# Kernel optimization log

Measured on AMD Instinct MI355X. Metric: run time of the kernel, lower is better.

The kernel has to match this reference:

```python
import jax, jax.numpy as jnp
import numpy as np


def _silu(x):
    return x * jax.nn.sigmoid(x)


def _mamba_dir(h, W_in, conv_w, conv_b, Wx, Wdt, bdt, A_log, Dp, W_out):
    """One unidirectional Mamba (v1) block. h: [B, L, Dm] -> [B, L, Dm]."""
    Bsz, L, Dm = h.shape
    Di = W_in.shape[0] // 2
    N = A_log.shape[1]
    K = conv_w.shape[1]
    dt_rank = Wdt.shape[1]
    # input projection -> x, z gates
    xz = jnp.einsum('bld,ed->ble', h, W_in)  # [B, L, 2*Di]
    x, z = xz[..., :Di], xz[..., Di:]
    # causal depthwise conv over time
    xc = jnp.transpose(x, (0, 2, 1))  # [B, Di, L]
    xc = jax.lax.conv_general_dilated(
        xc, conv_w[:, None, :], window_strides=(1,), padding=[(K - 1, 0)],
        dimension_numbers=('NCH', 'OIH', 'NCH'), feature_group_count=Di)
    x = _silu(jnp.transpose(xc, (0, 2, 1)) + conv_b[None, None, :])  # [B, L, Di]
    # data-dependent dt, B, C
    x_dbl = jnp.einsum('bld,ed->ble', x, Wx)  # [B, L, dt_rank + 2N]
    dt = x_dbl[..., :dt_rank]
    Bm = x_dbl[..., dt_rank:dt_rank + N]      # [B, L, N]
    Cm = x_dbl[..., dt_rank + N:]             # [B, L, N]
    dt = jax.nn.softplus(jnp.einsum('blr,dr->bld', dt, Wdt) + bdt)  # [B, L, Di]
    A = -jnp.exp(A_log)                       # [Di, N]
    # ZOH discretization
    dA = jnp.exp(dt[..., None] * A)                     # [B, L, Di, N]
    dBx = (dt * x)[..., None] * Bm[:, :, None, :]       # [B, L, Di, N]

    def step(hc, inp):
        dA_t, dBx_t, C_t = inp
        hc = dA_t * hc + dBx_t                          # [B, Di, N]
        return hc, jnp.einsum('bdn,bn->bd', hc, C_t)

    h0 = jnp.zeros((Bsz, Di, N), dtype=x.dtype)
    _, ys = jax.lax.scan(step, h0, (jnp.moveaxis(dA, 1, 0),
                                    jnp.moveaxis(dBx, 1, 0),
                                    jnp.moveaxis(Cm, 1, 0)))
    y = jnp.moveaxis(ys, 0, 1) + x * Dp                  # [B, L, Di]
    y = y * _silu(z)
    return jnp.einsum('bld,ed->ble', y, W_out)           # [B, L, Dm]


def setup_inputs() -> dict:
    key = jax.random.key(0)
    ks = jax.random.split(key, 16)
    B, L, Dm = 1, 2048, 1024
    Di, N, Kc, R = 2048, 16, 4, 64
    s = 0.02
    inp = {
        'hidden_states': jax.random.normal(ks[0], (B, L, Dm), jnp.float32),
        'W_in':  jax.random.normal(ks[1], (2 * Di, Dm), jnp.float32) * s,
        'W_out': jax.random.normal(ks[2], (Dm, Di), jnp.float32) * s,
    }
    a_log = jnp.log(jnp.broadcast_to(jnp.arange(1, N + 1, dtype=jnp.float32), (Di, N)))
    for i, d in enumerate(['fwd', 'rev']):
        o = 3 + 6 * i
        inp[f'conv_w_{d}'] = jax.random.normal(ks[o + 0], (Di, Kc), jnp.float32) * 0.2
        inp[f'conv_b_{d}'] = jnp.zeros((Di,), jnp.float32)
        inp[f'Wx_{d}']     = jax.random.normal(ks[o + 1], (R + 2 * N, Di), jnp.float32) * s
        inp[f'Wdt_{d}']    = jax.random.normal(ks[o + 2], (Di, R), jnp.float32) * s
        inp[f'bdt_{d}']    = jnp.full((Di,), -4.6, jnp.float32)  # softplus ~ 0.01
        inp[f'A_log_{d}']  = a_log
        inp[f'D_{d}']      = jnp.ones((Di,), jnp.float32)
    return inp


def reference(hidden_states, W_in, W_out,
              conv_w_fwd, conv_b_fwd, Wx_fwd, Wdt_fwd, bdt_fwd, A_log_fwd, D_fwd,
              conv_w_rev, conv_b_rev, Wx_rev, Wdt_rev, bdt_rev, A_log_rev, D_rev):
    out = _mamba_dir(hidden_states, W_in, conv_w_fwd, conv_b_fwd, Wx_fwd,
                     Wdt_fwd, bdt_fwd, A_log_fwd, D_fwd, W_out)
    h_rev = jnp.flip(hidden_states, axis=-2)
    out_rev = _mamba_dir(h_rev, W_in, conv_w_rev, conv_b_rev, Wx_rev,
                         Wdt_rev, bdt_rev, A_log_rev, D_rev, W_out)
    return out + jnp.flip(out_rev, axis=-2)
```

## Files before the change

kernel.cpp:

```cpp
#include <hip/hip_runtime.h>

#define L_LEN 2048
#define DM 1024
#define DI 2048
#define NS 16
#define KC 4
#define RR 64
#define XS 128
#define SPK 8
#define CH2 64
#define TCH2 (L_LEN / CH2)

typedef __attribute__((ext_vector_type(8))) short bf16x8;
typedef __attribute__((ext_vector_type(4))) float f32x4;

__device__ __forceinline__ float silu_f(float v) { return v / (1.f + __expf(-v)); }

__device__ __forceinline__ unsigned short f2bf(float f) {
  unsigned int u = __float_as_uint(f);
  u = (u + 0x7FFFu + ((u >> 16) & 1u)) >> 16;
  return (unsigned short)u;
}
__device__ __forceinline__ float bf2f(unsigned short u) {
  return __uint_as_float((unsigned int)u << 16);
}

#define GLOAD_LDS16(gptr, lptr)                                                \
  __builtin_amdgcn_global_load_lds(                                            \
      (const __attribute__((address_space(1))) void*)(gptr),                   \
      (__attribute__((address_space(3))) void*)(lptr), 16, 0, 0)

template <int BM, int EPI, int KSPLIT>
__global__ __launch_bounds__(256) void gemm_bf16(
    const unsigned short* __restrict__ A, const unsigned short* __restrict__ B,
    void* __restrict__ Cv, void* __restrict__ Cv2, int M, int N, int K,
    size_t zsA, size_t zsB, size_t zsC,
    const float* __restrict__ biasf, const float* __restrict__ biasr)
{
  constexpr int MF = BM / 32;
  constexpr int WM = BM / 2;
  A += (size_t)blockIdx.z * zsA;
  B += (size_t)blockIdx.z * zsB;
  __shared__ unsigned short smem[(BM + 128) * 32];
  unsigned short* As = smem;
  unsigned short* Bs = smem + BM * 32;
  const int tid = threadIdx.x;
  const int wid = tid >> 6;
  const int lane = tid & 63;
  const int bm = blockIdx.x * BM;
  const int bn = (KSPLIT > 1) ? 0 : blockIdx.y * 128;
  int kbeg = 0, kend = K;
  if (KSPLIT > 1) {
    int kl = K / KSPLIT;
    kbeg = blockIdx.y * kl; kend = kbeg + kl;
  }
  const int wm = wid >> 1, wn = wid & 1;
  const int arow = tid >> 2;
  const int swz_kel = (((tid & 3) ^ ((tid >> 3) & 3)) << 3);
  const int qa = (((lane >> 4) ^ ((lane >> 1) & 3)) << 4);
  const int frow = lane & 15;

  f32x4 acc[MF][4];
#pragma unroll
  for (int mi = 0; mi < MF; ++mi)
#pragma unroll
    for (int ni = 0; ni < 4; ++ni) acc[mi][ni] = 0.f;

  const unsigned short* Ab = A + (size_t)bm * K + swz_kel;
  const unsigned short* Bb = B + (size_t)bn * K + swz_kel;

  for (int k0 = kbeg; k0 < kend; k0 += 32) {
#pragma unroll
    for (int i = 0; i < BM / 64; ++i)
      GLOAD_LDS16(Ab + (size_t)(i * 64 + arow) * K + k0,
                  (char*)As + i * 4096 + wid * 1024);
#pragma unroll
    for (int i = 0; i < 2; ++i)
      GLOAD_LDS16(Bb + (size_t)(i * 64 + arow) * K + k0,
                  (char*)Bs + i * 4096 + wid * 1024);
    __syncthreads();
    bf16x8 af[MF], bfr[4];
#pragma unroll
    for (int mi = 0; mi < MF; ++mi)
      af[mi] = *(const bf16x8*)((const char*)As + (wm * WM + mi * 16 + frow) * 64 + qa);
#pragma unroll
    for (int ni = 0; ni < 4; ++ni)
      bfr[ni] = *(const bf16x8*)((const char*)Bs + (wn * 64 + ni * 16 + frow) * 64 + qa);
#pragma unroll
    for (int mi = 0; mi < MF; ++mi)
#pragma unroll
      for (int ni = 0; ni < 4; ++ni)
        acc[mi][ni] = __builtin_amdgcn_mfma_f32_16x16x32_bf16(
            af[mi], bfr[ni], acc[mi][ni], 0, 0, 0);
    __syncthreads();
  }
  const int crow0 = bm + wm * WM + ((lane >> 4) << 2);
  const int ccol0 = bn + wn * 64 + frow;
  if (EPI == 1) {
    unsigned short* Cu = (unsigned short*)Cv + (size_t)blockIdx.z * zsC;
    const float* bias = blockIdx.z ? biasr : biasf;
    float bn4[4];
#pragma unroll
    for (int ni = 0; ni < 4; ++ni) bn4[ni] = bias[ccol0 + ni * 16];
#pragma unroll
    for (int mi = 0; mi < MF; ++mi)
#pragma unroll
      for (int ni = 0; ni < 4; ++ni)
#pragma unroll
        for (int v = 0; v < 4; ++v) {
          float val = acc[mi][ni][v] + bn4[ni];
          float sp = (val > 20.f) ? val : __logf(1.f + __expf(val));
          Cu[(size_t)(crow0 + mi * 16 + v) * N + ccol0 + ni * 16] = f2bf(sp);
        }
  } else if (EPI == 2) {
    unsigned short* Co = (bn < DI) ? (unsigned short*)Cv : (unsigned short*)Cv2;
    const int cbase = (bn < DI) ? 0 : DI;
#pragma unroll
    for (int mi = 0; mi < MF; ++mi)
#pragma unroll
      for (int ni = 0; ni < 4; ++ni)
#pragma unroll
        for (int v = 0; v < 4; ++v)
          Co[(size_t)(crow0 + mi * 16 + v) * DI + ccol0 + ni * 16 - cbase] =
              f2bf(acc[mi][ni][v]);
  } else {
    float* Cf = (float*)Cv + (size_t)blockIdx.z * zsC;
    if (KSPLIT > 1) Cf += (size_t)blockIdx.y * 2 * M * 128;
#pragma unroll
    for (int mi = 0; mi < MF; ++mi)
#pragma unroll
      for (int ni = 0; ni < 4; ++ni)
#pragma unroll
        for (int v = 0; v < 4; ++v)
          Cf[(size_t)(crow0 + mi * 16 + v) * N + ccol0 + ni * 16] = acc[mi][ni][v];
  }
}

__global__ __launch_bounds__(256) void cast_all(
    const float* __restrict__ Wxf, const float* __restrict__ Wxr,
    const float* __restrict__ Wdtf, const float* __restrict__ Wdtr,
    const float* __restrict__ W_out, const float* __restrict__ h,
    const float* __restrict__ W_in,
    unsigned short* __restrict__ Wxpad, unsigned short* __restrict__ wdtb,
    unsigned short* __restrict__ wob, unsigned short* __restrict__ hb)
{
  int idx = (blockIdx.x * 256 + threadIdx.x) * 4;
  const int N0 = 2 * XS * DI;
  const int N1 = N0 + 2 * DI * RR;
  const int N2 = N1 + DM * DI;
  const int N3 = N2 + L_LEN * DM;
  float4 v;
  ushort4 o = {0, 0, 0, 0};
  if (idx < N0) {
    int dir = idx >> 18;
    int rem = idx & ((1 << 18) - 1);
    int row = rem >> 11;
    if (row < 96) {
      v = *(const float4*)((dir ? Wxr : Wxf) + (size_t)row * DI + (rem & (DI - 1)));
      o.x = f2bf(v.x); o.y = f2bf(v.y); o.z = f2bf(v.z); o.w = f2bf(v.w);
    }
    *(ushort4*)(Wxpad + idx) = o;
    return;
  }
  unsigned short* dst;
  const float* src;
  int j;
  if (idx < N1)      { j = idx - N0; int dir = j >> 17;
                       src = (dir ? Wdtr : Wdtf) + (j & ((1 << 17) - 1)) - (j & ~((1 << 17) - 1)) + (j & ~((1 << 17) - 1));
                       src = (dir ? Wdtr : Wdtf) + (j & ((1 << 17) - 1)); dst = wdtb + j; }
  else if (idx < N2) { j = idx - N1; src = W_out + j; dst = wob + j; }
  else if (idx < N3) { j = idx - N2; src = h + j;     dst = hb + j; }
  else               { j = idx - N3; src = W_in + j;  dst = hb + (L_LEN * DM) + j; }
  v = *(const float4*)src;
  o.x = f2bf(v.x); o.y = f2bf(v.y); o.z = f2bf(v.z); o.w = f2bf(v.w);
  *(ushort4*)dst = o;
}

__global__ __launch_bounds__(256) void xdbl_reduce2(
    const float* __restrict__ part, float* __restrict__ xdbl2,
    unsigned short* __restrict__ xdblb)
{
  int idx = (blockIdx.x * 256 + threadIdx.x) * 4;
  f32x4 s = {0.f, 0.f, 0.f, 0.f};
#pragma unroll
  for (int sp = 0; sp < SPK; ++sp) {
    f32x4 p = *(const f32x4*)(part + (size_t)sp * 2 * L_LEN * XS + idx);
#pragma unroll
    for (int j = 0; j < 4; ++j) s[j] += p[j];
  }
  *(f32x4*)(xdbl2 + idx) = s;
  int col = idx & (XS - 1);
  if (col < RR) {
    int dr = idx >> 7;
    ushort4 o;
    o.x = f2bf(s[0]); o.y = f2bf(s[1]); o.z = f2bf(s[2]); o.w = f2bf(s[3]);
    *(ushort4*)(xdblb + (size_t)dr * RR + col) = o;
  }
}

__global__ __launch_bounds__(256) void conv_silu4(
    const unsigned short* __restrict__ xb,
    const float* __restrict__ wf, const float* __restrict__ bf,
    const float* __restrict__ wr, const float* __restrict__ br,
    unsigned short* __restrict__ xob)
{
  const int dir = blockIdx.y;
  const int idx = (blockIdx.x * 256 + threadIdx.x) * 4;
  const int d = idx & (DI - 1);
  const int t = idx >> 11;
  const float* w = dir ? wr : wf;
  const float* bb = dir ? br : bf;
  f32x4 wq[4];
#pragma unroll
  for (int j = 0; j < 4; ++j) wq[j] = *(const f32x4*)(w + (d + j) * KC);
  f32x4 s = {0.f, 0.f, 0.f, 0.f};
#pragma unroll
  for (int k = 0; k < KC; ++k) {
    int tt = t - (KC - 1) + k;
    if (tt >= 0) {
      int row = dir ? (L_LEN - 1 - tt) : tt;
      ushort4 xv = *(const ushort4*)(xb + (size_t)row * DI + d);
      s[0] = fmaf(wq[0][k], bf2f(xv.x), s[0]);
      s[1] = fmaf(wq[1][k], bf2f(xv.y), s[1]);
      s[2] = fmaf(wq[2][k], bf2f(xv.z), s[2]);
      s[3] = fmaf(wq[3][k], bf2f(xv.w), s[3]);
    }
  }
  f32x4 bv = *(const f32x4*)(bb + d);
  ushort4 o;
  o.x = f2bf(silu_f(s[0] + bv[0])); o.y = f2bf(silu_f(s[1] + bv[1]));
  o.z = f2bf(silu_f(s[2] + bv[2])); o.w = f2bf(silu_f(s[3] + bv[3]));
  *(ushort4*)(xob + (size_t)dir * L_LEN * DI + idx) = o;
}

__global__ __launch_bounds__(256) void scan_partial2(
    const unsigned short* __restrict__ dtb16, const unsigned short* __restrict__ xwb,
    const float* __restrict__ xdbl2,
    const float* __restrict__ Alogf, const float* __restrict__ Alogr,
    float* __restrict__ hch, float* __restrict__ sdtb)
{
  const int dir = blockIdx.z, c = blockIdx.y;
  const int d = blockIdx.x * 256 + threadIdx.x;
  const int t0 = c * TCH2;
  const unsigned short* dtp = dtb16 + (size_t)dir * L_LEN * DI + (size_t)t0 * DI + d;
  const unsigned short* xp  = xwb   + (size_t)dir * L_LEN * DI + (size_t)t0 * DI + d;
  const float* xdp = xdbl2 + (size_t)dir * L_LEN * XS + (size_t)t0 * XS;
  const float* Alog = (dir ? Alogr : Alogf) + (size_t)d * NS;
  f32x4 a4[4], h4[4];
#pragma unroll
  for (int g = 0; g < 4; ++g) {
    f32x4 al = *(const f32x4*)(Alog + g * 4);
#pragma unroll
    for (int j = 0; j < 4; ++j) a4[g][j] = -__expf(al[j]);
    h4[g] = 0.f;
  }
  float sdt = 0.f;
#pragma unroll 4
  for (int tt = 0; tt < TCH2; ++tt) {
    float dtv = bf2f(*dtp);
    float xv  = bf2f(*xp);
    float dtx = dtv * xv;
    sdt += dtv;
#pragma unroll
    for (int g = 0; g < 4; ++g) {
      f32x4 Bv = *(const f32x4*)(xdp + RR + g * 4);
#pragma unroll
      for (int j = 0; j < 4; ++j)
        h4[g][j] = fmaf(__expf(dtv * a4[g][j]), h4[g][j], dtx * Bv[j]);
    }
    dtp += DI; xp += DI; xdp += XS;
  }
  float* hp = hch + ((((size_t)c * 2 + dir) * 4) * DI + d) * 4;
#pragma unroll
  for (int g = 0; g < 4; ++g) *(f32x4*)(hp + (size_t)g * DI * 4) = h4[g];
  sdtb[((size_t)c * 2 + dir) * DI + d] = sdt;
}

__global__ __launch_bounds__(256) void scan_combine2(
    float* __restrict__ hch, const float* __restrict__ sdtb,
    const float* __restrict__ Alogf, const float* __restrict__ Alogr)
{
  const int idx = blockIdx.x * 256 + threadIdx.x;
  const int dir = idx / (DI * NS);
  const int rem = idx - dir * (DI * NS);
  const int d = rem >> 4, n = rem & 15;
  const float* Alog = dir ? Alogr : Alogf;
  const float A = -__expf(Alog[rem]);
  float H = 0.f;
  for (int c = 0; c < CH2; ++c) {
    size_t off = ((((size_t)c * 2 + dir) * 4 + (n >> 2)) * DI + d) * 4 + (n & 3);
    float hc = hch[off];
    hch[off] = H;
    H = fmaf(__expf(A * sdtb[((size_t)c * 2 + dir) * DI + d]), H, hc);
  }
}

__global__ __launch_bounds__(256) void scan_final3(
    const unsigned short* __restrict__ dtb16, const unsigned short* __restrict__ xwb,
    const float* __restrict__ xdbl2,
    const float* __restrict__ Alogf, const float* __restrict__ Alogr,
    const float* __restrict__ Df, const float* __restrict__ Dr,
    const float* __restrict__ Hin, const unsigned short* __restrict__ zb,
    unsigned short* __restrict__ yb)
{
  __shared__ float ur_s[TCH2][256];
  const int c = blockIdx.y;
  const int d = blockIdx.x * 256 + threadIdx.x;
  const int tid = threadIdx.x;
  {
    const int cr = CH2 - 1 - c;
    const int tr0 = cr * TCH2;
    const unsigned short* dtp = dtb16 + (size_t)L_LEN * DI + (size_t)tr0 * DI + d;
    const unsigned short* xp  = xwb   + (size_t)L_LEN * DI + (size_t)tr0 * DI + d;
    const float* xdp = xdbl2 + (size_t)L_LEN * XS + (size_t)tr0 * XS;
    const float* Alog = Alogr + (size_t)d * NS;
    const float Dp = Dr[d];
    f32x4 a4[4], h4[4];
#pragma unroll
    for (int g = 0; g < 4; ++g) {
      f32x4 al = *(const f32x4*)(Alog + g * 4);
      h4[g] = *(const f32x4*)(Hin + ((((size_t)cr * 2 + 1) * 4 + g) * DI + d) * 4);
#pragma unroll
      for (int j = 0; j < 4; ++j) a4[g][j] = -__expf(al[j]);
    }
#pragma unroll 4
    for (int s = 0; s < TCH2; ++s) {
      float dtv = bf2f(*dtp);
      float xv  = bf2f(*xp);
      float dtx = dtv * xv;
      f32x4 p4 = {0.f, 0.f, 0.f, 0.f};
#pragma unroll
      for (int g = 0; g < 4; ++g) {
        f32x4 Bv = *(const f32x4*)(xdp + RR + g * 4);
        f32x4 Cv = *(const f32x4*)(xdp + RR + NS + g * 4);
#pragma unroll
        for (int j = 0; j < 4; ++j) {
          h4[g][j] = fmaf(__expf(dtv * a4[g][j]), h4[g][j], dtx * Bv[j]);
          p4[j] = fmaf(h4[g][j], Cv[j], p4[j]);
        }
      }
      float p = (p4[0] + p4[1]) + (p4[2] + p4[3]);
      ur_s[s][tid] = fmaf(xv, Dp, p);
      dtp += DI; xp += DI; xdp += XS;
    }
  }
  {
    const int t0 = c * TCH2;
    const unsigned short* dtp = dtb16 + (size_t)t0 * DI + d;
    const unsigned short* xp  = xwb   + (size_t)t0 * DI + d;
    const float* xdp = xdbl2 + (size_t)t0 * XS;
    const unsigned short* zp = zb + (size_t)t0 * DI + d;
    unsigned short* yp = yb + (size_t)t0 * DI + d;
    const float* Alog = Alogf + (size_t)d * NS;
    const float Dp = Df[d];
    f32x4 a4[4], h4[4];
#pragma unroll
    for (int g = 0; g < 4; ++g) {
      f32x4 al = *(const f32x4*)(Alog + g * 4);
      h4[g] = *(const f32x4*)(Hin + ((((size_t)c * 2 + 0) * 4 + g) * DI + d) * 4);
#pragma unroll
      for (int j = 0; j < 4; ++j) a4[g][j] = -__expf(al[j]);
    }
#pragma unroll 4
    for (int tt = 0; tt < TCH2; ++tt) {
      float dtv = bf2f(*dtp);
      float xv  = bf2f(*xp);
      float dtx = dtv * xv;
      f32x4 p4 = {0.f, 0.f, 0.f, 0.f};
#pragma unroll
      for (int g = 0; g < 4; ++g) {
        f32x4 Bv = *(const f32x4*)(xdp + RR + g * 4);
        f32x4 Cv = *(const f32x4*)(xdp + RR + NS + g * 4);
#pragma unroll
        for (int j = 0; j < 4; ++j) {
          h4[g][j] = fmaf(__expf(dtv * a4[g][j]), h4[g][j], dtx * Bv[j]);
          p4[j] = fmaf(h4[g][j], Cv[j], p4[j]);
        }
      }
      float p = (p4[0] + p4[1]) + (p4[2] + p4[3]);
      float uf = fmaf(xv, Dp, p);
      float u = uf + ur_s[TCH2 - 1 - tt][tid];
      float z = bf2f(*zp);
      *yp = f2bf(u * silu_f(z));
      dtp += DI; xp += DI; xdp += XS; zp += DI; yp += DI;
    }
  }
}

extern "C" void kernel_launch(void* const* d_in, const int* in_sizes, int n_in,
                              void* d_out, int out_size, void* d_ws, size_t ws_size,
                              hipStream_t stream)
{
  const float* h     = (const float*)d_in[0];
  const float* W_in  = (const float*)d_in[1];
  const float* W_out = (const float*)d_in[2];
  const float* cwf   = (const float*)d_in[3];
  const float* cbf   = (const float*)d_in[4];
  const float* Wxf   = (const float*)d_in[5];
  const float* Wdtf  = (const float*)d_in[6];
  const float* bdtf  = (const float*)d_in[7];
  const float* Alogf = (const float*)d_in[8];
  const float* Df    = (const float*)d_in[9];
  const float* cwr   = (const float*)d_in[10];
  const float* cbr   = (const float*)d_in[11];
  const float* Wxr   = (const float*)d_in[12];
  const float* Wdtr  = (const float*)d_in[13];
  const float* bdtr  = (const float*)d_in[14];
  const float* Alogr = (const float*)d_in[15];
  const float* Dr    = (const float*)d_in[16];

  float* ws = (float*)d_ws;
  size_t o = 0;
  float* xb_f    = ws + o; o += (size_t)L_LEN * DI / 2;
  float* zb_f    = ws + o; o += (size_t)L_LEN * DI / 2;
  float* xwb_f   = ws + o; o += (size_t)L_LEN * DI;
  float* dtb_f   = ws + o; o += (size_t)L_LEN * DI;
  float* xdbl2   = ws + o; o += 2ull * L_LEN * XS;
  float* xdblb_f = ws + o; o += (size_t)L_LEN * RR;
  float* wdtb_f  = ws + o; o += (size_t)DI * RR;
  float* Wxpad_f = ws + o; o += (size_t)XS * DI;
  float* wob_f   = ws + o; o += (size_t)DM * DI / 2;
  float* yb_f    = ws + o; o += (size_t)L_LEN * DI / 2;
  float* R0      = ws + o; o += 4456448;
  if (ws_size < o * sizeof(float)) return;

  unsigned short* xb    = (unsigned short*)xb_f;
  unsigned short* zb    = (unsigned short*)zb_f;
  unsigned short* xwb   = (unsigned short*)xwb_f;
  unsigned short* dtb16 = (unsigned short*)dtb_f;
  unsigned short* xdblb = (unsigned short*)xdblb_f;
  unsigned short* wdtb  = (unsigned short*)wdtb_f;
  unsigned short* Wxpad = (unsigned short*)Wxpad_f;
  unsigned short* wob   = (unsigned short*)wob_f;
  unsigned short* yb    = (unsigned short*)yb_f;

  unsigned short* hb   = (unsigned short*)R0;
  float*          part = R0;
  float*          hch  = R0;
  float*          sdtb = R0 + 4194304;

  cast_all<<<(2 * XS * DI + 2 * DI * RR + DM * DI + L_LEN * DM + 2 * DI * DM) / 1024,
             256, 0, stream>>>(
      Wxf, Wxr, Wdtf, Wdtr, W_out, h, W_in, Wxpad, wdtb, wob, hb);

  gemm_bf16<128, 2, 1><<<dim3(L_LEN / 128, (2 * DI) / 128, 1), 256, 0, stream>>>(
      hb, hb + (size_t)L_LEN * DM, xb, zb, L_LEN, 2 * DI, DM, 0, 0, 0,
      nullptr, nullptr);

  conv_silu4<<<dim3(L_LEN * DI / 1024, 2), 256, 0, stream>>>(
      xb, cwf, cbf, cwr, cbr, xwb);

  gemm_bf16<128, 0, SPK><<<dim3(L_LEN / 128, SPK, 2), 256, 0, stream>>>(
      xwb, Wxpad, part, nullptr, L_LEN, XS, DI,
      (size_t)L_LEN * DI, (size_t)XS * DI, (size_t)L_LEN * XS,
      nullptr, nullptr);
  xdbl_reduce2<<<(2 * L_LEN * XS) / 1024, 256, 0, stream>>>(part, xdbl2, xdblb);

  gemm_bf16<128, 1, 1><<<dim3(L_LEN / 128, DI / 128, 2), 256, 0, stream>>>(
      xdblb, wdtb, dtb16, nullptr, L_LEN, DI, RR,
      (size_t)L_LEN * RR, (size_t)DI * RR, (size_t)L_LEN * DI,
      bdtf, bdtr);

  scan_partial2<<<dim3(DI / 256, CH2, 2), 256, 0, stream>>>(
      dtb16, xwb, xdbl2, Alogf, Alogr, hch, sdtb);
  scan_combine2<<<(2 * DI * NS) / 256, 256, 0, stream>>>(
      hch, sdtb, Alogf, Alogr);
  scan_final3<<<dim3(DI / 256, CH2, 1), 256, 0, stream>>>(
      dtb16, xwb, xdbl2, Alogf, Alogr, Df, Dr, hch, zb, yb);

  gemm_bf16<64, 0, 1><<<dim3(L_LEN / 64, DM / 128, 1), 256, 0, stream>>>(
      yb, wob, (float*)d_out, nullptr, L_LEN, DM, DI, 0, 0, 0, nullptr, nullptr);
}
```

Baseline: 196.4 us.

## Double scan chunk count, use native exp2, keep reverse outputs in registers

Doubles the number of time chunks in the chunked selective scan (16 steps per chunk instead of 32), giving more blocks for parallelism and fewer serial steps per thread, and enlarges the workspace for the larger chunk-state buffer. It replaces __expf with a raw v_exp_f32 (exp2) using A prescaled by log2(e), fully unrolls the short chunk loops, and moves the reverse-direction per-step outputs from shared memory into a register array. The combine kernel now walks twice as many chunks serially, and the register array raises register pressure, which may reduce occupancy.

```diff
diff --git a/kernel.cpp b/kernel.cpp
--- a/kernel.cpp
+++ b/kernel.cpp
@@ -8,13 +8,19 @@
 #define RR 64
 #define XS 128
 #define SPK 8
-#define CH2 64
+#define CH2 128
 #define TCH2 (L_LEN / CH2)
 
 typedef __attribute__((ext_vector_type(8))) short bf16x8;
 typedef __attribute__((ext_vector_type(4))) float f32x4;
 
 __device__ __forceinline__ float silu_f(float v) { return v / (1.f + __expf(-v)); }
+
+__device__ __forceinline__ float exp2_f(float x) {
+  float r;
+  asm("v_exp_f32 %0, %1" : "=v"(r) : "v"(x));
+  return r;
+}
 
 __device__ __forceinline__ unsigned short f2bf(float f) {
   unsigned int u = __float_as_uint(f);
@@ -166,7 +172,6 @@
   const float* src;
   int j;
   if (idx < N1)      { j = idx - N0; int dir = j >> 17;
-                       src = (dir ? Wdtr : Wdtf) + (j & ((1 << 17) - 1)) - (j & ~((1 << 17) - 1)) + (j & ~((1 << 17) - 1));
                        src = (dir ? Wdtr : Wdtf) + (j & ((1 << 17) - 1)); dst = wdtb + j; }
   else if (idx < N2) { j = idx - N1; src = W_out + j; dst = wob + j; }
   else if (idx < N3) { j = idx - N2; src = h + j;     dst = hb + j; }
@@ -251,11 +256,11 @@
   for (int g = 0; g < 4; ++g) {
     f32x4 al = *(const f32x4*)(Alog + g * 4);
 #pragma unroll
-    for (int j = 0; j < 4; ++j) a4[g][j] = -__expf(al[j]);
+    for (int j = 0; j < 4; ++j) a4[g][j] = -__expf(al[j]) * 1.44269504f;
     h4[g] = 0.f;
   }
   float sdt = 0.f;
-#pragma unroll 4
+#pragma unroll
   for (int tt = 0; tt < TCH2; ++tt) {
     float dtv = bf2f(*dtp);
     float xv  = bf2f(*xp);
@@ -266,7 +271,7 @@
       f32x4 Bv = *(const f32x4*)(xdp + RR + g * 4);
 #pragma unroll
       for (int j = 0; j < 4; ++j)
-        h4[g][j] = fmaf(__expf(dtv * a4[g][j]), h4[g][j], dtx * Bv[j]);
+        h4[g][j] = fmaf(exp2_f(dtv * a4[g][j]), h4[g][j], dtx * Bv[j]);
     }
     dtp += DI; xp += DI; xdp += XS;
   }
@@ -285,13 +290,13 @@
   const int rem = idx - dir * (DI * NS);
   const int d = rem >> 4, n = rem & 15;
   const float* Alog = dir ? Alogr : Alogf;
-  const float A = -__expf(Alog[rem]);
+  const float A2 = -__expf(Alog[rem]) * 1.44269504f;
   float H = 0.f;
   for (int c = 0; c < CH2; ++c) {
     size_t off = ((((size_t)c * 2 + dir) * 4 + (n >> 2)) * DI + d) * 4 + (n & 3);
     float hc = hch[off];
     hch[off] = H;
-    H = fmaf(__expf(A * sdtb[((size_t)c * 2 + dir) * DI + d]), H, hc);
+    H = fmaf(exp2_f(A2 * sdtb[((size_t)c * 2 + dir) * DI + d]), H, hc);
   }
 }
 
@@ -303,10 +308,9 @@
     const float* __restrict__ Hin, const unsigned short* __restrict__ zb,
     unsigned short* __restrict__ yb)
 {
-  __shared__ float ur_s[TCH2][256];
   const int c = blockIdx.y;
   const int d = blockIdx.x * 256 + threadIdx.x;
-  const int tid = threadIdx.x;
+  float ur[TCH2];
   {
     const int cr = CH2 - 1 - c;
     const int tr0 = cr * TCH2;
@@ -321,9 +325,9 @@
       f32x4 al = *(const f32x4*)(Alog + g * 4);
       h4[g] = *(const f32x4*)(Hin + ((((size_t)cr * 2 + 1) * 4 + g) * DI + d) * 4);
 #pragma unroll
-      for (int j = 0; j < 4; ++j) a4[g][j] = -__expf(al[j]);
-    }
-#pragma unroll 4
+      for (int j = 0; j < 4; ++j) a4[g][j] = -__expf(al[j]) * 1.44269504f;
+    }
+#pragma unroll
     for (int s = 0; s < TCH2; ++s) {
       float dtv = bf2f(*dtp);
       float xv  = bf2f(*xp);
@@ -335,12 +339,12 @@
         f32x4 Cv = *(const f32x4*)(xdp + RR + NS + g * 4);
 #pragma unroll
         for (int j = 0; j < 4; ++j) {
-          h4[g][j] = fmaf(__expf(dtv * a4[g][j]), h4[g][j], dtx * Bv[j]);
+          h4[g][j] = fmaf(exp2_f(dtv * a4[g][j]), h4[g][j], dtx * Bv[j]);
           p4[j] = fmaf(h4[g][j], Cv[j], p4[j]);
         }
       }
       float p = (p4[0] + p4[1]) + (p4[2] + p4[3]);
-      ur_s[s][tid] = fmaf(xv, Dp, p);
+      ur[s] = fmaf(xv, Dp, p);
       dtp += DI; xp += DI; xdp += XS;
     }
   }
@@ -359,9 +363,9 @@
       f32x4 al = *(const f32x4*)(Alog + g * 4);
       h4[g] = *(const f32x4*)(Hin + ((((size_t)c * 2 + 0) * 4 + g) * DI + d) * 4);
 #pragma unroll
-      for (int j = 0; j < 4; ++j) a4[g][j] = -__expf(al[j]);
-    }
-#pragma unroll 4
+      for (int j = 0; j < 4; ++j) a4[g][j] = -__expf(al[j]) * 1.44269504f;
+    }
+#pragma unroll
     for (int tt = 0; tt < TCH2; ++tt) {
       float dtv = bf2f(*dtp);
       float xv  = bf2f(*xp);
@@ -373,13 +377,13 @@
         f32x4 Cv = *(const f32x4*)(xdp + RR + NS + g * 4);
 #pragma unroll
         for (int j = 0; j < 4; ++j) {
-          h4[g][j] = fmaf(__expf(dtv * a4[g][j]), h4[g][j], dtx * Bv[j]);
+          h4[g][j] = fmaf(exp2_f(dtv * a4[g][j]), h4[g][j], dtx * Bv[j]);
           p4[j] = fmaf(h4[g][j], Cv[j], p4[j]);
         }
       }
       float p = (p4[0] + p4[1]) + (p4[2] + p4[3]);
       float uf = fmaf(xv, Dp, p);
-      float u = uf + ur_s[TCH2 - 1 - tt][tid];
+      float u = uf + ur[TCH2 - 1 - tt];
       float z = bf2f(*zp);
       *yp = f2bf(u * silu_f(z));
       dtp += DI; xp += DI; xdp += XS; zp += DI; yp += DI;
@@ -421,7 +425,7 @@
   float* Wxpad_f = ws + o; o += (size_t)XS * DI;
   float* wob_f   = ws + o; o += (size_t)DM * DI / 2;
   float* yb_f    = ws + o; o += (size_t)L_LEN * DI / 2;
-  float* R0      = ws + o; o += 4456448;
+  float* R0      = ws + o; o += 8912896;
   if (ws_size < o * sizeof(float)) return;
 
   unsigned short* xb    = (unsigned short*)xb_f;
@@ -437,7 +441,7 @@
   unsigned short* hb   = (unsigned short*)R0;
   float*          part = R0;
   float*          hch  = R0;
-  float*          sdtb = R0 + 4194304;
+  float*          sdtb = R0 + 8388608;
 
   cast_all<<<(2 * XS * DI + 2 * DI * RR + DM * DI + L_LEN * DM + 2 * DI * DM) / 1024,
              256, 0, stream>>>(
```

Measured after the change: 192.9 us. Within noise of the previous version (-1.8%).
